# Performance work log

Hardware: AMD Instinct MI355X
Metric: run time of the kernel (lower is better)

Reference implementation:

```python
import jax, jax.numpy as jnp
import numpy as np

N = 4096

def setup_inputs() -> dict:
    key = jax.random.key(0)
    k1, k2, k3 = jax.random.split(key, 3)
    x = jax.random.normal(k1, (N, N), dtype=jnp.float32)
    # nn.Linear(N, N, bias=False) weight matrices, shape [out, in] = [N, N]
    s = 1.0 / np.sqrt(N)
    W_r = jax.random.uniform(k2, (N, N), dtype=jnp.float32, minval=-s, maxval=s)
    W_i = jax.random.uniform(k3, (N, N), dtype=jnp.float32, minval=-s, maxval=s)
    return {"x": x, "W_r": W_r, "W_i": W_i}

def reference(x, W_r, W_i):
    # Row pass: fft_in_rows[i] = Linear_real(x[i]) + 1j * Linear_imag(x[i])
    #   => R = x @ W_r^T + 1j * (x @ W_i^T)
    R_r = x @ W_r.T            # [N, N]
    R_i = x @ W_i.T            # [N, N]
    # Column pass: fft_in_cols[:, i] = fft_in_rows[:, i] @ (W_r + 1j W_i)
    #   => C = W^T @ R with W = W_r + 1j W_i (complex matmul in real arithmetic)
    C_r = W_r.T @ R_r - W_i.T @ R_i
    C_i = W_r.T @ R_i + W_i.T @ R_r
    # res = cat([real, imag], dim=1) -> [N, 2N]
    return jnp.concatenate([C_r, C_i], axis=1)
```

## Files before the change

### kernel.cpp

```cpp
#include <hip/hip_runtime.h>
#include <hip/hip_bf16.h>

#define NN 4096

typedef unsigned short u16;
using bf16x8 = __attribute__((ext_vector_type(8))) short;
using f32x4  = __attribute__((ext_vector_type(4))) float;
using u32x4  = __attribute__((ext_vector_type(4))) unsigned int;

__device__ inline u16 f2bf(float f) {
    union { float f; unsigned u; } c; c.f = f;
    unsigned r = (c.u + 0x7fffu + ((c.u >> 16) & 1u)) >> 16;
    return (u16)r;
}

__device__ inline void gld16(const void* g, void* l) {
    __builtin_amdgcn_global_load_lds(
        (const __attribute__((address_space(1))) void*)g,
        (__attribute__((address_space(3))) void*)l, 16, 0, 0);
}

__device__ inline bf16x8 negbf(bf16x8 v) {
    u32x4 u; __builtin_memcpy(&u, &v, 16);
    u ^= 0x80008000u;
    bf16x8 r; __builtin_memcpy(&r, &u, 16);
    return r;
}

__global__ __launch_bounds__(256) void cvt_bf16(const float* __restrict__ s,
                                                u16* __restrict__ d) {
    size_t i = ((size_t)blockIdx.x * 256 + threadIdx.x) * 8;
    float4 v0 = *(const float4*)(s + i);
    float4 v1 = *(const float4*)(s + i + 4);
    bf16x8 o;
    o[0] = (short)f2bf(v0.x); o[1] = (short)f2bf(v0.y);
    o[2] = (short)f2bf(v0.z); o[3] = (short)f2bf(v0.w);
    o[4] = (short)f2bf(v1.x); o[5] = (short)f2bf(v1.y);
    o[6] = (short)f2bf(v1.z); o[7] = (short)f2bf(v1.w);
    *(bf16x8*)(d + i) = o;
}

__global__ __launch_bounds__(256) void tr_cvt(const float* __restrict__ s,
                                              u16* __restrict__ d) {
    __shared__ float t[32][33];
    int x  = blockIdx.x * 32 + threadIdx.x;
    int y0 = blockIdx.y * 32;
#pragma unroll
    for (int j = 0; j < 32; j += 8)
        t[threadIdx.y + j][threadIdx.x] = s[(size_t)(y0 + threadIdx.y + j) * NN + x];
    __syncthreads();
    int x2 = blockIdx.y * 32 + threadIdx.x;
    int y2 = blockIdx.x * 32;
#pragma unroll
    for (int j = 0; j < 32; j += 8)
        d[(size_t)(y2 + threadIdx.y + j) * NN + x2] = f2bf(t[threadIdx.x][threadIdx.y + j]);
}

__global__ __launch_bounds__(256) void gemm_nt_dual(
    const u16* __restrict__ A0, const u16* __restrict__ A1,
    const u16* __restrict__ B,
    u16* __restrict__ C0, u16* __restrict__ C1) {
    __shared__ u16 lA[128 * 32];
    __shared__ u16 lB[128 * 32];
    const u16* A = blockIdx.z ? A1 : A0;
    u16*       C = blockIdx.z ? C1 : C0;

    const int tid  = threadIdx.x;
    const int lane = tid & 63;
    const int wid  = tid >> 6;
    const int wm   = (wid >> 1) * 64;
    const int wn   = (wid & 1) * 64;
    const int brow = blockIdx.y * 128;
    const int bcol = blockIdx.x * 128;

    f32x4 acc[4][4] = {};

    const int r0 = tid >> 2;
    const int c0 = (tid & 3) * 8;
    const size_t aoff0 = (size_t)(brow + r0) * NN + c0;
    const size_t aoff1 = aoff0 + (size_t)64 * NN;
    const size_t boff0 = (size_t)(bcol + r0) * NN + c0;
    const size_t boff1 = boff0 + (size_t)64 * NN;
    const int rl = lane & 15;
    const int kg = (lane >> 4) * 8;

    for (int kk = 0; kk < NN; kk += 32) {
        gld16(A + aoff0 + kk, &lA[tid * 8]);
        gld16(A + aoff1 + kk, &lA[2048 + tid * 8]);
        gld16(B + boff0 + kk, &lB[tid * 8]);
        gld16(B + boff1 + kk, &lB[2048 + tid * 8]);
        __syncthreads();
        bf16x8 a[4], b[4];
#pragma unroll
        for (int i = 0; i < 4; i++)
            a[i] = *(const bf16x8*)&lA[(wm + i * 16 + rl) * 32 + kg];
#pragma unroll
        for (int j = 0; j < 4; j++)
            b[j] = *(const bf16x8*)&lB[(wn + j * 16 + rl) * 32 + kg];
#pragma unroll
        for (int i = 0; i < 4; i++)
#pragma unroll
            for (int j = 0; j < 4; j++)
                acc[i][j] = __builtin_amdgcn_mfma_f32_16x16x32_bf16(a[i], b[j], acc[i][j], 0, 0, 0);
        __syncthreads();
    }

    const int rg = (lane >> 4) * 4;
#pragma unroll
    for (int i = 0; i < 4; i++)
#pragma unroll
        for (int j = 0; j < 4; j++) {
            int col = bcol + wn + j * 16 + rl;
#pragma unroll
            for (int r = 0; r < 4; r++) {
                int row = brow + wm + i * 16 + rg + r;
                C[(size_t)row * NN + col] = f2bf(acc[i][j][r]);
            }
        }
}

__global__ __launch_bounds__(256, 2) void gemm_pass2(
    const u16* __restrict__ Ar, const u16* __restrict__ Ai,
    const u16* __restrict__ Br, const u16* __restrict__ Bi,
    float* __restrict__ Out) {
    __shared__ u16 lAr[128 * 32];
    __shared__ u16 lAi[128 * 32];
    __shared__ u16 lBr[128 * 32];
    __shared__ u16 lBi[128 * 32];

    const int tid  = threadIdx.x;
    const int lane = tid & 63;
    const int wid  = tid >> 6;
    const int wm   = (wid >> 1) * 64;
    const int wn   = (wid & 1) * 64;
    const int brow = blockIdx.y * 128;
    const int bcol = blockIdx.x * 128;

    f32x4 accr[4][4] = {};
    f32x4 acci[4][4] = {};

    const int r0 = tid >> 2;
    const int c0 = (tid & 3) * 8;
    const size_t moff0 = (size_t)(brow + r0) * NN + c0;
    const size_t moff1 = moff0 + (size_t)64 * NN;
    const size_t noff0 = (size_t)(bcol + r0) * NN + c0;
    const size_t noff1 = noff0 + (size_t)64 * NN;
    const int rl = lane & 15;
    const int kg = (lane >> 4) * 8;

    for (int kk = 0; kk < NN; kk += 32) {
        gld16(Ar + moff0 + kk, &lAr[tid * 8]);
        gld16(Ar + moff1 + kk, &lAr[2048 + tid * 8]);
        gld16(Ai + moff0 + kk, &lAi[tid * 8]);
        gld16(Ai + moff1 + kk, &lAi[2048 + tid * 8]);
        gld16(Br + noff0 + kk, &lBr[tid * 8]);
        gld16(Br + noff1 + kk, &lBr[2048 + tid * 8]);
        gld16(Bi + noff0 + kk, &lBi[tid * 8]);
        gld16(Bi + noff1 + kk, &lBi[2048 + tid * 8]);
        __syncthreads();
        bf16x8 ar[4], ai[4], br[4], bi[4];
#pragma unroll
        for (int i = 0; i < 4; i++) {
            ar[i] = *(const bf16x8*)&lAr[(wm + i * 16 + rl) * 32 + kg];
            ai[i] = *(const bf16x8*)&lAi[(wm + i * 16 + rl) * 32 + kg];
        }
#pragma unroll
        for (int j = 0; j < 4; j++) {
            br[j] = *(const bf16x8*)&lBr[(wn + j * 16 + rl) * 32 + kg];
            bi[j] = *(const bf16x8*)&lBi[(wn + j * 16 + rl) * 32 + kg];
        }
#pragma unroll
        for (int i = 0; i < 4; i++)
#pragma unroll
            for (int j = 0; j < 4; j++) {
                acci[i][j] = __builtin_amdgcn_mfma_f32_16x16x32_bf16(ar[i], bi[j], acci[i][j], 0, 0, 0);
                acci[i][j] = __builtin_amdgcn_mfma_f32_16x16x32_bf16(ai[i], br[j], acci[i][j], 0, 0, 0);
            }
#pragma unroll
        for (int i = 0; i < 4; i++) ai[i] = negbf(ai[i]);
#pragma unroll
        for (int i = 0; i < 4; i++)
#pragma unroll
            for (int j = 0; j < 4; j++) {
                accr[i][j] = __builtin_amdgcn_mfma_f32_16x16x32_bf16(ar[i], br[j], accr[i][j], 0, 0, 0);
                accr[i][j] = __builtin_amdgcn_mfma_f32_16x16x32_bf16(ai[i], bi[j], accr[i][j], 0, 0, 0);
            }
        __syncthreads();
    }

    const int rg = (lane >> 4) * 4;
#pragma unroll
    for (int i = 0; i < 4; i++)
#pragma unroll
        for (int j = 0; j < 4; j++) {
            int col = bcol + wn + j * 16 + rl;
#pragma unroll
            for (int r = 0; r < 4; r++) {
                int row = brow + wm + i * 16 + rg + r;
                Out[(size_t)row * (2 * NN) + col]      = accr[i][j][r];
                Out[(size_t)row * (2 * NN) + NN + col] = acci[i][j][r];
            }
        }
}

extern "C" void kernel_launch(void* const* d_in, const int* in_sizes, int n_in,
                              void* d_out, int out_size, void* d_ws, size_t ws_size,
                              hipStream_t stream) {
    const float* x  = (const float*)d_in[0];
    const float* Wr = (const float*)d_in[1];
    const float* Wi = (const float*)d_in[2];
    float* out = (float*)d_out;

    const size_t SZ = (size_t)NN * NN;
    u16* ws  = (u16*)d_ws;
    u16* xb  = ws;
    u16* Wrb = ws + SZ;
    u16* Wib = ws + 2 * SZ;
    u16* Rtr = ws + 3 * SZ;
    u16* Rti = ws + 4 * SZ;

    cvt_bf16<<<8192, 256, 0, stream>>>(x,  xb);
    cvt_bf16<<<8192, 256, 0, stream>>>(Wr, Wrb);
    cvt_bf16<<<8192, 256, 0, stream>>>(Wi, Wib);

    gemm_nt_dual<<<dim3(32, 32, 2), 256, 0, stream>>>(Wrb, Wib, xb, Rtr, Rti);

    u16* WrT = xb;
    u16* WiT = Wrb;
    tr_cvt<<<dim3(128, 128), dim3(32, 8), 0, stream>>>(Wr, WrT);
    tr_cvt<<<dim3(128, 128), dim3(32, 8), 0, stream>>>(Wi, WiT);

    gemm_pass2<<<dim3(32, 32), 256, 0, stream>>>(WrT, WiT, Rtr, Rti, out);
}
```

Before: 831.9 us.

## Double-buffer LDS tiles and XOR-swizzle layout in both GEMM kernels

Both GEMM kernels now keep two LDS stages, so the global-to-LDS loads for the next k-slice are issued before the MFMAs on the current one. The barrier count drops from two per iteration to one. The global source column is also XOR-swizzled by row, with a matching swizzled read offset, to cut LDS bank conflicts on the 16-byte fragment reads. The cost is doubled shared memory: 64KB in pass2, which may limit occupancy against its launch bound of two blocks per CU.

```diff
diff --git a/kernel.cpp b/kernel.cpp
--- a/kernel.cpp
+++ b/kernel.cpp
@@ -56,12 +56,12 @@
         d[(size_t)(y2 + threadIdx.y + j) * NN + x2] = f2bf(t[threadIdx.x][threadIdx.y + j]);
 }
 
+
 __global__ __launch_bounds__(256) void gemm_nt_dual(
     const u16* __restrict__ A0, const u16* __restrict__ A1,
     const u16* __restrict__ B,
     u16* __restrict__ C0, u16* __restrict__ C1) {
-    __shared__ u16 lA[128 * 32];
-    __shared__ u16 lB[128 * 32];
+    __shared__ u16 sm[2][2][4096];
     const u16* A = blockIdx.z ? A1 : A0;
     u16*       C = blockIdx.z ? C1 : C0;
 
@@ -76,57 +76,67 @@
     f32x4 acc[4][4] = {};
 
     const int r0 = tid >> 2;
-    const int c0 = (tid & 3) * 8;
-    const size_t aoff0 = (size_t)(brow + r0) * NN + c0;
+    const int lb = (tid & 3) ^ ((r0 >> 1) & 3);
+    const size_t aoff0 = (size_t)(brow + r0) * NN + lb * 8;
     const size_t aoff1 = aoff0 + (size_t)64 * NN;
-    const size_t boff0 = (size_t)(bcol + r0) * NN + c0;
+    const size_t boff0 = (size_t)(bcol + r0) * NN + lb * 8;
     const size_t boff1 = boff0 + (size_t)64 * NN;
     const int rl = lane & 15;
-    const int kg = (lane >> 4) * 8;
-
-    for (int kk = 0; kk < NN; kk += 32) {
-        gld16(A + aoff0 + kk, &lA[tid * 8]);
-        gld16(A + aoff1 + kk, &lA[2048 + tid * 8]);
-        gld16(B + boff0 + kk, &lB[tid * 8]);
-        gld16(B + boff1 + kk, &lB[2048 + tid * 8]);
-        __syncthreads();
+    const int kg = (((lane >> 4) ^ ((rl >> 1) & 3))) * 8;
+
+#define STAGE1(buf, kk) do { \
+    gld16(A + aoff0 + (kk), &sm[buf][0][tid * 8]); \
+    gld16(A + aoff1 + (kk), &sm[buf][0][2048 + tid * 8]); \
+    gld16(B + boff0 + (kk), &sm[buf][1][tid * 8]); \
+    gld16(B + boff1 + (kk), &sm[buf][1][2048 + tid * 8]); \
+} while (0)
+
+    auto compute = [&](int buf) {
         bf16x8 a[4], b[4];
 #pragma unroll
         for (int i = 0; i < 4; i++)
-            a[i] = *(const bf16x8*)&lA[(wm + i * 16 + rl) * 32 + kg];
+            a[i] = *(const bf16x8*)&sm[buf][0][(wm + i * 16 + rl) * 32 + kg];
 #pragma unroll
         for (int j = 0; j < 4; j++)
-            b[j] = *(const bf16x8*)&lB[(wn + j * 16 + rl) * 32 + kg];
+            b[j] = *(const bf16x8*)&sm[buf][1][(wn + j * 16 + rl) * 32 + kg];
 #pragma unroll
         for (int i = 0; i < 4; i++)
 #pragma unroll
             for (int j = 0; j < 4; j++)
                 acc[i][j] = __builtin_amdgcn_mfma_f32_16x16x32_bf16(a[i], b[j], acc[i][j], 0, 0, 0);
+    };
+
+    STAGE1(0, 0);
+    __syncthreads();
+    int cur = 0;
+    for (int t = 0; t < NN / 32 - 1; t++) {
+        STAGE1(cur ^ 1, (t + 1) * 32);
+        compute(cur);
         __syncthreads();
+        cur ^= 1;
     }
+    compute(cur);
 
     const int rg = (lane >> 4) * 4;
 #pragma unroll
     for (int i = 0; i < 4; i++)
 #pragma unroll
         for (int j = 0; j < 4; j++) {
-            int col = bcol + wn + j * 16 + rl;
+            int col = bcol + wn + j * 16 + (lane & 15);
 #pragma unroll
             for (int r = 0; r < 4; r++) {
                 int row = brow + wm + i * 16 + rg + r;
                 C[(size_t)row * NN + col] = f2bf(acc[i][j][r]);
             }
         }
+#undef STAGE1
 }
 
 __global__ __launch_bounds__(256, 2) void gemm_pass2(
     const u16* __restrict__ Ar, const u16* __restrict__ Ai,
     const u16* __restrict__ Br, const u16* __restrict__ Bi,
     float* __restrict__ Out) {
-    __shared__ u16 lAr[128 * 32];
-    __shared__ u16 lAi[128 * 32];
-    __shared__ u16 lBr[128 * 32];
-    __shared__ u16 lBi[128 * 32];
+    __shared__ u16 sm[2][4][4096];
 
     const int tid  = threadIdx.x;
     const int lane = tid & 63;
@@ -140,34 +150,36 @@
     f32x4 acci[4][4] = {};
 
     const int r0 = tid >> 2;
-    const int c0 = (tid & 3) * 8;
-    const size_t moff0 = (size_t)(brow + r0) * NN + c0;
+    const int lb = (tid & 3) ^ ((r0 >> 1) & 3);
+    const size_t moff0 = (size_t)(brow + r0) * NN + lb * 8;
     const size_t moff1 = moff0 + (size_t)64 * NN;
-    const size_t noff0 = (size_t)(bcol + r0) * NN + c0;
+    const size_t noff0 = (size_t)(bcol + r0) * NN + lb * 8;
     const size_t noff1 = noff0 + (size_t)64 * NN;
     const int rl = lane & 15;
-    const int kg = (lane >> 4) * 8;
-
-    for (int kk = 0; kk < NN; kk += 32) {
-        gld16(Ar + moff0 + kk, &lAr[tid * 8]);
-        gld16(Ar + moff1 + kk, &lAr[2048 + tid * 8]);
-        gld16(Ai + moff0 + kk, &lAi[tid * 8]);
-        gld16(Ai + moff1 + kk, &lAi[2048 + tid * 8]);
-        gld16(Br + noff0 + kk, &lBr[tid * 8]);
-        gld16(Br + noff1 + kk, &lBr[2048 + tid * 8]);
-        gld16(Bi + noff0 + kk, &lBi[tid * 8]);
-        gld16(Bi + noff1 + kk, &lBi[2048 + tid * 8]);
-        __syncthreads();
+    const int kg = (((lane >> 4) ^ ((rl >> 1) & 3))) * 8;
+
+#define STAGE2(buf, kk) do { \
+    gld16(Ar + moff0 + (kk), &sm[buf][0][tid * 8]); \
+    gld16(Ar + moff1 + (kk), &sm[buf][0][2048 + tid * 8]); \
+    gld16(Ai + moff0 + (kk), &sm[buf][1][tid * 8]); \
+    gld16(Ai + moff1 + (kk), &sm[buf][1][2048 + tid * 8]); \
+    gld16(Br + noff0 + (kk), &sm[buf][2][tid * 8]); \
+    gld16(Br + noff1 + (kk), &sm[buf][2][2048 + tid * 8]); \
+    gld16(Bi + noff0 + (kk), &sm[buf][3][tid * 8]); \
+    gld16(Bi + noff1 + (kk), &sm[buf][3][2048 + tid * 8]); \
+} while (0)
+
+    auto compute = [&](int buf) {
         bf16x8 ar[4], ai[4], br[4], bi[4];
 #pragma unroll
         for (int i = 0; i < 4; i++) {
-            ar[i] = *(const bf16x8*)&lAr[(wm + i * 16 + rl) * 32 + kg];
-            ai[i] = *(const bf16x8*)&lAi[(wm + i * 16 + rl) * 32 + kg];
+            ar[i] = *(const bf16x8*)&sm[buf][0][(wm + i * 16 + rl) * 32 + kg];
+            ai[i] = *(const bf16x8*)&sm[buf][1][(wm + i * 16 + rl) * 32 + kg];
         }
 #pragma unroll
         for (int j = 0; j < 4; j++) {
-            br[j] = *(const bf16x8*)&lBr[(wn + j * 16 + rl) * 32 + kg];
-            bi[j] = *(const bf16x8*)&lBi[(wn + j * 16 + rl) * 32 + kg];
+            br[j] = *(const bf16x8*)&sm[buf][2][(wn + j * 16 + rl) * 32 + kg];
+            bi[j] = *(const bf16x8*)&sm[buf][3][(wn + j * 16 + rl) * 32 + kg];
         }
 #pragma unroll
         for (int i = 0; i < 4; i++)
@@ -185,15 +197,25 @@
                 accr[i][j] = __builtin_amdgcn_mfma_f32_16x16x32_bf16(ar[i], br[j], accr[i][j], 0, 0, 0);
                 accr[i][j] = __builtin_amdgcn_mfma_f32_16x16x32_bf16(ai[i], bi[j], accr[i][j], 0, 0, 0);
             }
+    };
+
+    STAGE2(0, 0);
+    __syncthreads();
+    int cur = 0;
+    for (int t = 0; t < NN / 32 - 1; t++) {
+        STAGE2(cur ^ 1, (t + 1) * 32);
+        compute(cur);
         __syncthreads();
+        cur ^= 1;
     }
+    compute(cur);
 
     const int rg = (lane >> 4) * 4;
 #pragma unroll
     for (int i = 0; i < 4; i++)
 #pragma unroll
         for (int j = 0; j < 4; j++) {
-            int col = bcol + wn + j * 16 + rl;
+            int col = bcol + wn + j * 16 + (lane & 15);
 #pragma unroll
             for (int r = 0; r < 4; r++) {
                 int row = brow + wm + i * 16 + rg + r;
@@ -201,6 +223,7 @@
                 Out[(size_t)row * (2 * NN) + NN + col] = acci[i][j][r];
             }
         }
+#undef STAGE2
 }
 
 extern "C" void kernel_launch(void* const* d_in, const int* in_sizes, int n_in,
```

Measured after the change: 870.5 us. 1.05x slower.
